# Kernel tuning notes

Hardware: AMD Instinct MI355X
Metric: run time of the kernel (lower is better)

## Reference

```python
import itertools
import jax, jax.numpy as jnp
import numpy as np

B = 16384
LATENT = 16
F = 6
DIMS = [1000000, 500000, 500000, 100000, 10000, 1000]
SEQ_LENS = [1, 1, 50, 20, 1, 1]


def setup_inputs() -> dict:
    key = jax.random.key(0)
    ks = jax.random.split(key, 32)
    inp = {}
    for i in range(F):
        inp[f"x{i}"] = jax.random.randint(ks[i], (B, SEQ_LENS[i]), 0, DIMS[i], dtype=jnp.int32)
    for i in range(F):
        # stacked FFM tables for field i: slot s corresponds to target field j (j != i)
        inp[f"E{i}"] = 0.01 * jax.random.normal(ks[6 + i], (F - 1, DIMS[i], LATENT), dtype=jnp.float32)
        inp[f"L{i}"] = 0.01 * jax.random.normal(ks[12 + i], (DIMS[i], 1), dtype=jnp.float32)
    inp["Wd"] = 0.1 * jax.random.normal(ks[20], (F, 1), dtype=jnp.float32)
    inp["bd"] = jnp.zeros((1,), dtype=jnp.float32)
    return inp


def _forward(xs, Es, Ls, Wd, bd):
    def pair_emb(i, j):
        # table named "i-j" in the original: field i's vocab, specialized for target field j
        slot = j - 1 if j > i else j
        e = Es[i][slot][xs[i]]          # [B, L_i, latent]
        return jnp.mean(e, axis=1)      # [B, latent] (mean over seq; L_i==1 for non-seq)

    fm = jnp.zeros((xs[0].shape[0],), dtype=Es[0].dtype)
    for i, j in itertools.combinations(range(F), 2):
        fm = fm + jnp.sum(pair_emb(i, j) * pair_emb(j, i), axis=-1)  # [B]
    fm = fm[:, None]                                                 # [B, 1]

    # linear term: 1-dim embedding per field, mean-pooled, concat -> Dense(1, relu)
    feats = jnp.concatenate([jnp.mean(Ls[i][xs[i]], axis=1) for i in range(F)], axis=1)  # [B, F]
    lin = jax.nn.relu(feats @ Wd + bd)  # [B, 1]
    return jax.nn.sigmoid(lin + fm)


def reference(x0, x1, x2, x3, x4, x5, E0, E1, E2, E3, E4, E5, L0, L1, L2, L3, L4, L5, Wd, bd):
    xs = [x0, x1, x2, x3, x4, x5]
    Es = [E0, E1, E2, E3, E4, E5]
    Ls = [L0, L1, L2, L3, L4, L5]
    return _forward(xs, Es, Ls, Wd, bd)
```

## Files before the change

### kernel.cpp

```cpp
#include <hip/hip_runtime.h>
#include <math.h>

#define BATCH 16384
#define LATENT 16


template<int SEQ, int DIM>
__device__ __forceinline__ void field_accum(const int* __restrict__ x,
                                            const float* __restrict__ E,
                                            const float* __restrict__ L,
                                            int b, int t,
                                            float v[5], float& lmean)
{
    const size_t slotStride = (size_t)DIM * LATENT;
    float a0 = 0.f, a1 = 0.f, a2 = 0.f, a3 = 0.f, a4 = 0.f, ls = 0.f;
#pragma unroll 2
    for (int s = 0; s < SEQ; ++s) {
        const int idx = x[b * SEQ + s];
        const size_t off = (size_t)idx * LATENT + t;
        a0 += E[off];
        a1 += E[off + slotStride];
        a2 += E[off + 2 * slotStride];
        a3 += E[off + 3 * slotStride];
        a4 += E[off + 4 * slotStride];
        ls += L[idx];
    }
    const float inv = 1.0f / (float)SEQ;
    v[0] = a0 * inv; v[1] = a1 * inv; v[2] = a2 * inv;
    v[3] = a3 * inv; v[4] = a4 * inv;
    lmean = ls * inv;
}

__global__ __launch_bounds__(256) void ffm_kernel(
    const int* __restrict__ x0, const int* __restrict__ x1,
    const int* __restrict__ x2, const int* __restrict__ x3,
    const int* __restrict__ x4, const int* __restrict__ x5,
    const float* __restrict__ E0, const float* __restrict__ E1,
    const float* __restrict__ E2, const float* __restrict__ E3,
    const float* __restrict__ E4, const float* __restrict__ E5,
    const float* __restrict__ L0, const float* __restrict__ L1,
    const float* __restrict__ L2, const float* __restrict__ L3,
    const float* __restrict__ L4, const float* __restrict__ L5,
    const float* __restrict__ Wd, const float* __restrict__ bd,
    float* __restrict__ out)
{
    const int tid = blockIdx.x * blockDim.x + threadIdx.x;
    const int b = tid >> 4;
    const int t = tid & 15;

    float v0[5], v1[5], v2[5], v3[5], v4[5], v5[5];
    float f0, f1, f2, f3, f4, f5;

    field_accum<1, 1000000>(x0, E0, L0, b, t, v0, f0);
    field_accum<1,  500000>(x1, E1, L1, b, t, v1, f1);
    field_accum<50, 500000>(x2, E2, L2, b, t, v2, f2);
    field_accum<20, 100000>(x3, E3, L3, b, t, v3, f3);
    field_accum<1,   10000>(x4, E4, L4, b, t, v4, f4);
    field_accum<1,    1000>(x5, E5, L5, b, t, v5, f5);

    float fm = v0[0] * v1[0] + v0[1] * v2[0] + v0[2] * v3[0]
             + v0[3] * v4[0] + v0[4] * v5[0]
             + v1[1] * v2[1] + v1[2] * v3[1] + v1[3] * v4[1] + v1[4] * v5[1]
             + v2[2] * v3[2] + v2[3] * v4[2] + v2[4] * v5[2]
             + v3[3] * v4[3] + v3[4] * v5[3]
             + v4[4] * v5[4];

    fm += __shfl_xor(fm, 1, 16);
    fm += __shfl_xor(fm, 2, 16);
    fm += __shfl_xor(fm, 4, 16);
    fm += __shfl_xor(fm, 8, 16);

    if (t == 0) {
        float lin = f0 * Wd[0] + f1 * Wd[1] + f2 * Wd[2]
                  + f3 * Wd[3] + f4 * Wd[4] + f5 * Wd[5] + bd[0];
        lin = fmaxf(lin, 0.0f);
        const float z = lin + fm;
        out[b] = 1.0f / (1.0f + __expf(-z));
    }
}

extern "C" void kernel_launch(void* const* d_in, const int* in_sizes, int n_in,
                              void* d_out, int out_size, void* d_ws, size_t ws_size,
                              hipStream_t stream)
{
    const int* x0 = (const int*)d_in[0];
    const int* x1 = (const int*)d_in[1];
    const int* x2 = (const int*)d_in[2];
    const int* x3 = (const int*)d_in[3];
    const int* x4 = (const int*)d_in[4];
    const int* x5 = (const int*)d_in[5];

    const float *E0, *E1, *E2, *E3, *E4, *E5;
    const float *L0, *L1, *L2, *L3, *L4, *L5;

    if (in_sizes[7] == 1000000) {
        E0 = (const float*)d_in[6];  L0 = (const float*)d_in[7];
        E1 = (const float*)d_in[8];  L1 = (const float*)d_in[9];
        E2 = (const float*)d_in[10]; L2 = (const float*)d_in[11];
        E3 = (const float*)d_in[12]; L3 = (const float*)d_in[13];
        E4 = (const float*)d_in[14]; L4 = (const float*)d_in[15];
        E5 = (const float*)d_in[16]; L5 = (const float*)d_in[17];
    } else {
        E0 = (const float*)d_in[6];  E1 = (const float*)d_in[7];
        E2 = (const float*)d_in[8];  E3 = (const float*)d_in[9];
        E4 = (const float*)d_in[10]; E5 = (const float*)d_in[11];
        L0 = (const float*)d_in[12]; L1 = (const float*)d_in[13];
        L2 = (const float*)d_in[14]; L3 = (const float*)d_in[15];
        L4 = (const float*)d_in[16]; L5 = (const float*)d_in[17];
    }
    const float* Wd = (const float*)d_in[18];
    const float* bd = (const float*)d_in[19];
    float* out = (float*)d_out;

    dim3 block(256);
    dim3 grid((BATCH * LATENT) / 256);
    hipLaunchKernelGGL(ffm_kernel, grid, block, 0, stream,
                       x0, x1, x2, x3, x4, x5,
                       E0, E1, E2, E3, E4, E5,
                       L0, L1, L2, L3, L4, L5,
                       Wd, bd, out);
}
```

Before: 624.3 us.

## Vectorize embedding gathers to float4 and split sequence across lane groups

Each 16-lane group now loads four latent values per lane with 128-bit loads, and the four lane subgroups split the sequence positions of the pooled fields, reducing the partial sums with xor shuffles. Single-position fields take a direct gather path, and the pairwise dot products accumulate in vector form before a short final shuffle reduction. This is meant to cut the per-lane serial sequence loop and the number of load instructions. In exchange it adds extra shuffles, changes the floating-point summation order, and drops the 64-bit offset arithmetic.

```diff
diff --git a/kernel.cpp b/kernel.cpp
--- a/kernel.cpp
+++ b/kernel.cpp
@@ -5,30 +5,86 @@
 #define LATENT 16
 
 
+typedef float f4 __attribute__((ext_vector_type(4)));
+
+__device__ __forceinline__ float phsum(float v) {
+    v += __shfl_xor(v, 4, 16);
+    v += __shfl_xor(v, 8, 16);
+    return v;
+}
+__device__ __forceinline__ f4 phsum4(f4 a) {
+    a.x = phsum(a.x);
+    a.y = phsum(a.y);
+    a.z = phsum(a.z);
+    a.w = phsum(a.w);
+    return a;
+}
+
 template<int SEQ, int DIM>
-__device__ __forceinline__ void field_accum(const int* __restrict__ x,
+__device__ __forceinline__ void field_split(const int* __restrict__ x,
                                             const float* __restrict__ E,
                                             const float* __restrict__ L,
-                                            int b, int t,
-                                            float v[5], float& lmean)
+                                            int b, int voq, int h,
+                                            f4 v[5], float& lmean)
 {
-    const size_t slotStride = (size_t)DIM * LATENT;
-    float a0 = 0.f, a1 = 0.f, a2 = 0.f, a3 = 0.f, a4 = 0.f, ls = 0.f;
-#pragma unroll 2
-    for (int s = 0; s < SEQ; ++s) {
-        const int idx = x[b * SEQ + s];
-        const size_t off = (size_t)idx * LATENT + t;
-        a0 += E[off];
-        a1 += E[off + slotStride];
-        a2 += E[off + 2 * slotStride];
-        a3 += E[off + 3 * slotStride];
-        a4 += E[off + 4 * slotStride];
+    const float* __restrict__ e0 = E;
+    const float* __restrict__ e1 = E + (size_t)DIM * LATENT;
+    const float* __restrict__ e2 = E + (size_t)DIM * LATENT * 2;
+    const float* __restrict__ e3 = E + (size_t)DIM * LATENT * 3;
+    const float* __restrict__ e4 = E + (size_t)DIM * LATENT * 4;
+    const int* __restrict__ xb = x + b * SEQ + h;
+
+    f4 a0 = 0.f, a1 = 0.f, a2 = 0.f, a3 = 0.f, a4 = 0.f;
+    float ls = 0.f;
+    constexpr int K    = SEQ / 4;
+    constexpr int TAIL = SEQ & 3;
+#pragma unroll 4
+    for (int k = 0; k < K; ++k) {
+        const int idx = xb[4 * k];
+        const int off = idx * LATENT + voq;
+        a0 += *(const f4*)(e0 + off);
+        a1 += *(const f4*)(e1 + off);
+        a2 += *(const f4*)(e2 + off);
+        a3 += *(const f4*)(e3 + off);
+        a4 += *(const f4*)(e4 + off);
         ls += L[idx];
     }
+    if constexpr (TAIL > 0) {
+        if (h < TAIL) {
+            const int idx = xb[4 * K];
+            const int off = idx * LATENT + voq;
+            a0 += *(const f4*)(e0 + off);
+            a1 += *(const f4*)(e1 + off);
+            a2 += *(const f4*)(e2 + off);
+            a3 += *(const f4*)(e3 + off);
+            a4 += *(const f4*)(e4 + off);
+            ls += L[idx];
+        }
+    }
     const float inv = 1.0f / (float)SEQ;
-    v[0] = a0 * inv; v[1] = a1 * inv; v[2] = a2 * inv;
-    v[3] = a3 * inv; v[4] = a4 * inv;
-    lmean = ls * inv;
+    v[0] = phsum4(a0) * inv;
+    v[1] = phsum4(a1) * inv;
+    v[2] = phsum4(a2) * inv;
+    v[3] = phsum4(a3) * inv;
+    v[4] = phsum4(a4) * inv;
+    lmean = phsum(ls) * inv;
+}
+
+template<int DIM>
+__device__ __forceinline__ void field_one(const int* __restrict__ x,
+                                          const float* __restrict__ E,
+                                          const float* __restrict__ L,
+                                          int b, int voq,
+                                          f4 v[5], float& lmean)
+{
+    const int idx = x[b];
+    const int off = idx * LATENT + voq;
+    v[0] = *(const f4*)(E + off);
+    v[1] = *(const f4*)(E + (size_t)DIM * LATENT     + off);
+    v[2] = *(const f4*)(E + (size_t)DIM * LATENT * 2 + off);
+    v[3] = *(const f4*)(E + (size_t)DIM * LATENT * 3 + off);
+    v[4] = *(const f4*)(E + (size_t)DIM * LATENT * 4 + off);
+    lmean = L[idx];
 }
 
 __global__ __launch_bounds__(256) void ffm_kernel(
@@ -45,34 +101,41 @@
     float* __restrict__ out)
 {
     const int tid = blockIdx.x * blockDim.x + threadIdx.x;
-    const int b = tid >> 4;
-    const int t = tid & 15;
+    const int b   = tid >> 4;
+    const int t   = tid & 15;
+    const int q   = t & 3;
+    const int h   = t >> 2;
+    const int voq = q * 4;
 
-    float v0[5], v1[5], v2[5], v3[5], v4[5], v5[5];
-    float f0, f1, f2, f3, f4, f5;
+    f4 v0[5], v1[5], v2[5], v3[5], v4[5], v5[5];
+    float f0m, f1m, f2m, f3m, f4m, f5m;
+    f4 fmv = 0.f;
 
-    field_accum<1, 1000000>(x0, E0, L0, b, t, v0, f0);
-    field_accum<1,  500000>(x1, E1, L1, b, t, v1, f1);
-    field_accum<50, 500000>(x2, E2, L2, b, t, v2, f2);
-    field_accum<20, 100000>(x3, E3, L3, b, t, v3, f3);
-    field_accum<1,   10000>(x4, E4, L4, b, t, v4, f4);
-    field_accum<1,    1000>(x5, E5, L5, b, t, v5, f5);
+    field_split<50, 500000>(x2, E2, L2, b, voq, h, v2, f2m);
+    field_split<20, 100000>(x3, E3, L3, b, voq, h, v3, f3m);
+    fmv += v2[2] * v3[2];
 
-    float fm = v0[0] * v1[0] + v0[1] * v2[0] + v0[2] * v3[0]
-             + v0[3] * v4[0] + v0[4] * v5[0]
-             + v1[1] * v2[1] + v1[2] * v3[1] + v1[3] * v4[1] + v1[4] * v5[1]
-             + v2[2] * v3[2] + v2[3] * v4[2] + v2[4] * v5[2]
-             + v3[3] * v4[3] + v3[4] * v5[3]
-             + v4[4] * v5[4];
+    field_one<1000000>(x0, E0, L0, b, voq, v0, f0m);
+    fmv += v0[1] * v2[0] + v0[2] * v3[0];
 
-    fm += __shfl_xor(fm, 1, 16);
-    fm += __shfl_xor(fm, 2, 16);
-    fm += __shfl_xor(fm, 4, 16);
-    fm += __shfl_xor(fm, 8, 16);
+    field_one<500000>(x1, E1, L1, b, voq, v1, f1m);
+    fmv += v0[0] * v1[0] + v1[1] * v2[1] + v1[2] * v3[1];
+
+    field_one<10000>(x4, E4, L4, b, voq, v4, f4m);
+    fmv += v0[3] * v4[0] + v1[3] * v4[1]
+         + v2[3] * v4[2] + v3[3] * v4[3];
+
+    field_one<1000>(x5, E5, L5, b, voq, v5, f5m);
+    fmv += v0[4] * v5[0] + v1[4] * v5[1] + v2[4] * v5[2]
+         + v3[4] * v5[3] + v4[4] * v5[4];
+
+    float fm = fmv.x + fmv.y + fmv.z + fmv.w;
+    fm += __shfl_xor(fm, 1, 4);
+    fm += __shfl_xor(fm, 2, 4);
 
     if (t == 0) {
-        float lin = f0 * Wd[0] + f1 * Wd[1] + f2 * Wd[2]
-                  + f3 * Wd[3] + f4 * Wd[4] + f5 * Wd[5] + bd[0];
+        float lin = f0m * Wd[0] + f1m * Wd[1] + f2m * Wd[2]
+                  + f3m * Wd[3] + f4m * Wd[4] + f5m * Wd[5] + bd[0];
         lin = fmaxf(lin, 0.0f);
         const float z = lin + fm;
         out[b] = 1.0f / (1.0f + __expf(-z));
```

After: 619.0 us. Within noise of the previous version (-0.8%).
